# Optimization experiments

Measured on AMD Instinct MI355X. Metric: run time of the kernel, lower is better.

The kernel has to match this reference:

```python
import jax, jax.numpy as jnp
import numpy as np

R, K = 16, 64  # rel_size (heads), key_size (head dim)
LN_EPS = 1e-5


def apply_rope(x, pos):
    # pos: [B,S,1,K], halves are sin/cos; x: [B,S,R,K]
    sin, cos = jnp.split(pos, 2, axis=-1)
    x0, x1 = jnp.split(x, 2, axis=-1)
    return jnp.concatenate([x0 * cos - x1 * sin, x0 * sin + x1 * cos], axis=-1)


def setup_inputs() -> dict:
    key = jax.random.key(0)
    ks = jax.random.split(key, 6)
    B, S, H = 2, 2048, 1024
    x = jax.random.normal(ks[0], (B, S, H), dtype=jnp.float32)
    pos = jax.random.uniform(ks[1], (B, S, 1, K), dtype=jnp.float32)
    W_qkv = jax.random.normal(ks[2], (H, R * K * 3), dtype=jnp.float32) * (H ** -0.5)
    b_qkv = jax.random.normal(ks[3], (R * K * 3,), dtype=jnp.float32) * 0.02
    W_out = jax.random.normal(ks[4], (R * K, H), dtype=jnp.float32) * ((R * K) ** -0.5)
    b_out = jax.random.normal(ks[5], (H,), dtype=jnp.float32) * 0.02
    ln_g = jnp.ones((H,), dtype=jnp.float32)
    ln_b = jnp.zeros((H,), dtype=jnp.float32)
    return {"x": x, "pos": pos, "W_qkv": W_qkv, "b_qkv": b_qkv,
            "W_out": W_out, "b_out": b_out, "ln_g": ln_g, "ln_b": ln_b}


def reference(x, pos, W_qkv, b_qkv, W_out, b_out, ln_g, ln_b):
    B, S, H = x.shape
    qkv = (x @ W_qkv + b_qkv).reshape(B, S, R, 3 * K)
    q, k, v = jnp.split(qkv, 3, axis=-1)  # each [B,S,R,K]
    k = k / jnp.linalg.norm(k, axis=-1, keepdims=True)
    q = apply_rope(q, pos)
    k = apply_rope(k, pos)
    # SDPA with scale=1 (as in the original call)
    scores = jnp.einsum('bqhd,bkhd->bhqk', q, k)
    attn = jax.nn.softmax(scores, axis=-1)
    ctx = jnp.einsum('bhqk,bkhd->bqhd', attn, v).reshape(B, S, R * K)
    postx = ctx @ W_out + b_out
    y = x + postx
    mu = jnp.mean(y, axis=-1, keepdims=True)
    var = jnp.mean(jnp.square(y - mu), axis=-1, keepdims=True)
    return (y - mu) * jax.lax.rsqrt(var + LN_EPS) * ln_g + ln_b
```

## Files before the change

kernel.cpp:

```cpp
#include <hip/hip_runtime.h>


#define B_   2
#define S_   2048
#define H_   1024
#define R_   16
#define BS_  (B_*S_)
#define NQKV 3072
#define LOG2E 1.44269504088896f

typedef float    floatx4 __attribute__((ext_vector_type(4)));
typedef _Float16 half8   __attribute__((ext_vector_type(8)));
typedef _Float16 half4   __attribute__((ext_vector_type(4)));
typedef __fp16   fp16x2  __attribute__((ext_vector_type(2)));

__device__ __forceinline__ float exp2_raw(float x) {
#if __has_builtin(__builtin_amdgcn_exp2f)
    return __builtin_amdgcn_exp2f(x);
#else
    float r;
    asm("v_exp_f32 %0, %1\n\ts_nop 0" : "=v"(r) : "v"(x));
    return r;
#endif
}

__device__ __forceinline__ void gl_lds16(const _Float16* g, _Float16* l) {
    __builtin_amdgcn_global_load_lds(
        (const __attribute__((address_space(1))) unsigned int*)g,
        (__attribute__((address_space(3))) unsigned int*)l, 16, 0, 0);
}

__global__ __launch_bounds__(256) void prep0_kernel(
    const float* __restrict__ x, _Float16* __restrict__ x_h,
    const float* __restrict__ W_qkv, _Float16* __restrict__ wqkv_t,
    const float* __restrict__ W_out, _Float16* __restrict__ wout_t)
{
    __shared__ float tile[32][33];
    int bid = blockIdx.x, tid = threadIdx.x;
    if (bid < 4096) {
        int i = bid * 1024 + tid * 4;
        float4 v = *(const float4*)(x + i);
        half4 h;
        h.x = (_Float16)v.x; h.y = (_Float16)v.y;
        h.z = (_Float16)v.z; h.w = (_Float16)v.w;
        *(half4*)(x_h + i) = h;
        return;
    }
    const float* in; _Float16* out; int rows, cols, bx, by;
    if (bid < 7168) {
        int t = bid - 4096;
        in = W_qkv; out = wqkv_t; rows = H_; cols = NQKV;
        bx = t % 96; by = t / 96;
    } else {
        int t = bid - 7168;
        in = W_out; out = wout_t; rows = H_; cols = H_;
        bx = t & 31; by = t >> 5;
    }
    int cx = bx * 32, ry = by * 32;
    int tx = tid & 31, ty = tid >> 5;
#pragma unroll
    for (int i = 0; i < 32; i += 8)
        tile[ty + i][tx] = in[(size_t)(ry + ty + i) * cols + cx + tx];
    __syncthreads();
#pragma unroll
    for (int i = 0; i < 32; i += 8)
        out[(size_t)(cx + ty + i) * rows + ry + tx] = (_Float16)tile[tx][ty + i];
}

template <bool F16OUT>
__global__ __launch_bounds__(256) void gemm_f16_mfma(
    const _Float16* __restrict__ A, const _Float16* __restrict__ Bt,
    const float* __restrict__ bias, const float* __restrict__ resid,
    float* __restrict__ Cf, _Float16* __restrict__ Ch, int M, int N, int Kd)
{
    __shared__ _Float16 Als[2][4096];
    __shared__ _Float16 Bls[2][4096];
    int tid  = threadIdx.x;
    int lane = tid & 63, w = tid >> 6;
    int wr = w >> 1, wc = w & 1;
    int fr = lane & 15, fq = lane >> 4;
    int m0 = blockIdx.y * 128, n0 = blockIdx.x * 128;

    floatx4 acc[4][4] = {};

    const _Float16* ga[2]; const _Float16* gb[2];
    int loff[2];
#pragma unroll
    for (int i2 = 0; i2 < 2; ++i2) {
        int ch = 2 * w + i2;
        int row = ch * 16 + (lane >> 2), col = (lane & 3) * 8;
        ga[i2] = A  + (size_t)(m0 + row) * Kd + col;
        gb[i2] = Bt + (size_t)(n0 + row) * Kd + col;
        loff[i2] = ch * 512;
    }

    int nIter = Kd >> 5;
#pragma unroll
    for (int i2 = 0; i2 < 2; ++i2) {
        gl_lds16(ga[i2], &Als[0][loff[i2]]);
        gl_lds16(gb[i2], &Bls[0][loff[i2]]);
    }

    for (int it = 0; it < nIter; ++it) {
        int cur = it & 1;
        __syncthreads();
        if (it + 1 < nIter) {
            int k1 = (it + 1) << 5;
#pragma unroll
            for (int i2 = 0; i2 < 2; ++i2) {
                gl_lds16(ga[i2] + k1, &Als[cur ^ 1][loff[i2]]);
                gl_lds16(gb[i2] + k1, &Bls[cur ^ 1][loff[i2]]);
            }
        }
        const _Float16* Ab = Als[cur];
        const _Float16* Bb = Bls[cur];
        half8 af[4], bf[4];
#pragma unroll
        for (int i = 0; i < 4; ++i)
            af[i] = *(const half8*)(Ab + (wr * 64 + i * 16 + fr) * 32 + fq * 8);
#pragma unroll
        for (int j = 0; j < 4; ++j)
            bf[j] = *(const half8*)(Bb + (wc * 64 + j * 16 + fr) * 32 + fq * 8);
#pragma unroll
        for (int i = 0; i < 4; ++i)
#pragma unroll
            for (int j = 0; j < 4; ++j)
                acc[i][j] = __builtin_amdgcn_mfma_f32_16x16x32_f16(
                    af[i], bf[j], acc[i][j], 0, 0, 0);
    }

#pragma unroll
    for (int i = 0; i < 4; ++i)
#pragma unroll
        for (int j = 0; j < 4; ++j)
#pragma unroll
            for (int r2 = 0; r2 < 4; ++r2) {
                int row = m0 + wr * 64 + i * 16 + fq * 4 + r2;
                int col = n0 + wc * 64 + j * 16 + fr;
                float v = acc[i][j][r2] + bias[col];
                if constexpr (F16OUT) {
                    Ch[(size_t)row * N + col] = (_Float16)v;
                } else {
                    if (resid) v += resid[(size_t)row * N + col];
                    Cf[(size_t)row * N + col] = v;
                }
            }
}

__global__ __launch_bounds__(256) void prep1_kernel(
    const _Float16* __restrict__ qkvh, const float* __restrict__ pos,
    _Float16* __restrict__ qt, _Float16* __restrict__ kt,
    _Float16* __restrict__ vt2)
{
    __shared__ float tile[64][65];
    int head = blockIdx.x, tau = blockIdx.y;
    int s0 = tau * 64;
    int b = head >> 4, rh = head & 15;
    int lane = threadIdx.x & 63, w = threadIdx.x >> 6;

#pragma unroll
    for (int si = w; si < 64; si += 4)
        tile[si][lane] =
            (float)qkvh[(size_t)(b * S_ + s0 + si) * NQKV + rh * 192 + 128 + lane];
    __syncthreads();
    {
        int P = lane;
        int op = P >> 3;
        int hi = (P >> 2) & 1, lo = P & 3;
#pragma unroll
        for (int d = w; d < 64; d += 4) {
            int ol = op ^ (d & 7);
            int key = 32 * (ol >> 2) + 16 * hi + 4 * (ol & 3) + lo;
            vt2[(((size_t)head * 32 + tau) * 64 + d) * 64 + P] = (_Float16)tile[key][d];
        }
    }

    for (int i = 0; i < 16; ++i) {
        int s = s0 + w * 16 + i;
        int bs = b * S_ + s;
        const _Float16* base = qkvh + (size_t)bs * NQKV + rh * 192;
        float qv = (float)base[lane];
        float kv = (float)base[64 + lane];

        float ss = kv * kv;
#pragma unroll
        for (int off = 32; off > 0; off >>= 1) ss += __shfl_xor(ss, off);
        kv *= rsqrtf(ss);

        int j = lane & 31;
        float sn = pos[(size_t)bs * 64 + j];
        float cs = pos[(size_t)bs * 64 + 32 + j];
        float qp = __shfl_xor(qv, 32);
        float kp = __shfl_xor(kv, 32);
        float qo, ko;
        if (lane < 32) { qo = qv * cs - qp * sn; ko = kv * cs - kp * sn; }
        else           { qo = qp * sn + qv * cs; ko = kp * sn + kv * cs; }

        size_t oidx = ((size_t)head * S_ + s) * 64 + lane;
        qt[oidx] = (_Float16)(qo * LOG2E);
        kt[oidx] = (_Float16)ko;
    }
}

__global__ __launch_bounds__(256) void attn_mfma_kernel(
    const _Float16* __restrict__ qt, const _Float16* __restrict__ kt,
    const _Float16* __restrict__ vt2, _Float16* __restrict__ ctx)
{
    __shared__ _Float16 Kls[64 * 64];
    __shared__ _Float16 Vls[64 * 64];

    int head = blockIdx.x, q0 = blockIdx.y * 128;
    int b = head >> 4, rh = head & 15;
    int tid = threadIdx.x, lane = tid & 63, w = tid >> 6;
    int g = lane >> 4, c = lane & 15;

    half8 qf[2][2];
    float mL[2], l_s[2] = {0.f, 0.f};
#pragma unroll
    for (int qg = 0; qg < 2; ++qg) {
        const _Float16* qp =
            qt + ((size_t)head * S_ + q0 + w * 32 + qg * 16 + c) * 64 + 8 * g;
        qf[qg][0] = *(const half8*)qp;
        qf[qg][1] = *(const half8*)(qp + 32);
        float qq = 0.f;
#pragma unroll
        for (int i = 0; i < 8; ++i) {
            float a = (float)qf[qg][0][i], b2 = (float)qf[qg][1][i];
            qq += a * a + b2 * b2;
        }
        qq += __shfl_xor(qq, 16);
        qq += __shfl_xor(qq, 32);
        mL[qg] = sqrtf(qq);
    }

    floatx4 o_acc[2][4] = {};

    const _Float16* kg[2]; const _Float16* vg[2];
    _Float16 *kl_[2], *vl_[2];
#pragma unroll
    for (int i2 = 0; i2 < 2; ++i2) {
        int ch = 2 * w + i2;
        int krow = ch * 8 + (lane >> 3);
        int koct = (lane & 7) ^ (lane >> 3);
        kg[i2] = kt + ((size_t)head * S_ + krow) * 64 + koct * 8;
        kl_[i2] = Kls + ch * 512;
        vg[i2] = vt2 + ((size_t)head * 32) * 4096 + ch * 512 + lane * 8;
        vl_[i2] = Vls + ch * 512;
    }

    int co = c & 7;

    for (int j0 = 0; j0 < S_; j0 += 64) {
        __syncthreads();
#pragma unroll
        for (int i2 = 0; i2 < 2; ++i2) {
            gl_lds16(kg[i2] + (size_t)j0 * 64, kl_[i2]);
            gl_lds16(vg[i2] + (size_t)(j0 >> 6) * 4096, vl_[i2]);
        }
        __syncthreads();

        half8 kfr[8];
#pragma unroll
        for (int t = 0; t < 4; ++t) {
            const _Float16* krow = Kls + (16 * t + c) * 64;
            kfr[2 * t]     = *(const half8*)(krow + ((g) ^ co) * 8);
            kfr[2 * t + 1] = *(const half8*)(krow + ((4 + g) ^ co) * 8);
        }

        union { half8 v; fp16x2 h2[4]; } pf[2][2];
#pragma unroll
        for (int qg = 0; qg < 2; ++qg) {
            float negm = -mL[qg];
            floatx4 zinit = {negm, negm, negm, negm};
            floatx4 sacc[4];
#pragma unroll
            for (int t = 0; t < 4; ++t) {
                floatx4 z = zinit;
                z = __builtin_amdgcn_mfma_f32_16x16x32_f16(
                    kfr[2 * t], qf[qg][0], z, 0, 0, 0);
                z = __builtin_amdgcn_mfma_f32_16x16x32_f16(
                    kfr[2 * t + 1], qf[qg][1], z, 0, 0, 0);
                sacc[t] = z;
            }
            float ps = 0.f;
#pragma unroll
            for (int t = 0; t < 4; ++t)
#pragma unroll
                for (int r = 0; r < 4; ++r) {
                    float p = exp2_raw(sacc[t][r]);
                    sacc[t][r] = p;
                    ps += p;
                }
            l_s[qg] += ps;
            pf[qg][0].h2[0] = __builtin_amdgcn_cvt_pkrtz(sacc[0][0], sacc[0][1]);
            pf[qg][0].h2[1] = __builtin_amdgcn_cvt_pkrtz(sacc[0][2], sacc[0][3]);
            pf[qg][0].h2[2] = __builtin_amdgcn_cvt_pkrtz(sacc[1][0], sacc[1][1]);
            pf[qg][0].h2[3] = __builtin_amdgcn_cvt_pkrtz(sacc[1][2], sacc[1][3]);
            pf[qg][1].h2[0] = __builtin_amdgcn_cvt_pkrtz(sacc[2][0], sacc[2][1]);
            pf[qg][1].h2[1] = __builtin_amdgcn_cvt_pkrtz(sacc[2][2], sacc[2][3]);
            pf[qg][1].h2[2] = __builtin_amdgcn_cvt_pkrtz(sacc[3][0], sacc[3][1]);
            pf[qg][1].h2[3] = __builtin_amdgcn_cvt_pkrtz(sacc[3][2], sacc[3][3]);
        }

#pragma unroll
        for (int t = 0; t < 4; ++t) {
            const _Float16* vrow = Vls + (16 * t + c) * 64;
            half8 v0 = *(const half8*)(vrow + ((g) ^ co) * 8);
            half8 v1 = *(const half8*)(vrow + ((4 + g) ^ co) * 8);
#pragma unroll
            for (int qg = 0; qg < 2; ++qg) {
                o_acc[qg][t] = __builtin_amdgcn_mfma_f32_16x16x32_f16(
                    v0, pf[qg][0].v, o_acc[qg][t], 0, 0, 0);
                o_acc[qg][t] = __builtin_amdgcn_mfma_f32_16x16x32_f16(
                    v1, pf[qg][1].v, o_acc[qg][t], 0, 0, 0);
            }
        }
    }

#pragma unroll
    for (int qg = 0; qg < 2; ++qg) {
        float lt = l_s[qg];
        lt += __shfl_xor(lt, 16);
        lt += __shfl_xor(lt, 32);
        float inv = 1.f / lt;
        size_t rowbase =
            ((size_t)(b * S_ + q0 + w * 32 + qg * 16 + c)) * 1024 + rh * 64;
#pragma unroll
        for (int t = 0; t < 4; ++t) {
            union { half4 v; fp16x2 h2[2]; } e;
            e.h2[0] = __builtin_amdgcn_cvt_pkrtz(o_acc[qg][t][0] * inv,
                                                 o_acc[qg][t][1] * inv);
            e.h2[1] = __builtin_amdgcn_cvt_pkrtz(o_acc[qg][t][2] * inv,
                                                 o_acc[qg][t][3] * inv);
            *(half4*)(ctx + rowbase + 16 * t + 4 * g) = e.v;
        }
    }
}

__global__ __launch_bounds__(256) void ln_kernel(
    float* __restrict__ y, const float* __restrict__ g, const float* __restrict__ bb)
{
    int row = blockIdx.x, tid = threadIdx.x;
    float* p = y + (size_t)row * 1024;
    float4 v = ((const float4*)p)[tid];
    float sum = v.x + v.y + v.z + v.w;
    float sq  = v.x*v.x + v.y*v.y + v.z*v.z + v.w*v.w;
#pragma unroll
    for (int off = 32; off > 0; off >>= 1) {
        sum += __shfl_xor(sum, off);
        sq  += __shfl_xor(sq,  off);
    }
    __shared__ float rs[4], rq[4];
    int w = tid >> 6;
    if ((tid & 63) == 0) { rs[w] = sum; rq[w] = sq; }
    __syncthreads();
    sum = rs[0] + rs[1] + rs[2] + rs[3];
    sq  = rq[0] + rq[1] + rq[2] + rq[3];
    float mean = sum * (1.f / 1024.f);
    float var  = sq * (1.f / 1024.f) - mean * mean;
    float inv  = rsqrtf(var + 1e-5f);
    float4 gv = ((const float4*)g)[tid];
    float4 bv = ((const float4*)bb)[tid];
    v.x = (v.x - mean) * inv * gv.x + bv.x;
    v.y = (v.y - mean) * inv * gv.y + bv.y;
    v.z = (v.z - mean) * inv * gv.z + bv.z;
    v.w = (v.w - mean) * inv * gv.w + bv.w;
    ((float4*)p)[tid] = v;
}

extern "C" void kernel_launch(void* const* d_in, const int* in_sizes, int n_in,
                              void* d_out, int out_size, void* d_ws, size_t ws_size,
                              hipStream_t stream)
{
    const float* x     = (const float*)d_in[0];
    const float* pos   = (const float*)d_in[1];
    const float* W_qkv = (const float*)d_in[2];
    const float* b_qkv = (const float*)d_in[3];
    const float* W_out = (const float*)d_in[4];
    const float* b_out = (const float*)d_in[5];
    const float* ln_g  = (const float*)d_in[6];
    const float* ln_b  = (const float*)d_in[7];
    float* out = (float*)d_out;

    char* ws = (char*)d_ws;
    _Float16* x_h    = (_Float16*)(ws);
    _Float16* wqkv_t = (_Float16*)(ws + ((size_t)8  << 20));
    _Float16* wout_t = (_Float16*)(ws + ((size_t)14 << 20));
    _Float16* qkvh   = (_Float16*)(ws + ((size_t)16 << 20));
    _Float16* qt_h   = (_Float16*)(ws + ((size_t)40 << 20));
    _Float16* kt_h   = (_Float16*)(ws + ((size_t)48 << 20));
    _Float16* vt2_h  = (_Float16*)(ws + ((size_t)56 << 20));
    _Float16* ctx_h  = (_Float16*)(ws + ((size_t)64 << 20));

    prep0_kernel<<<8192, 256, 0, stream>>>(x, x_h, W_qkv, wqkv_t, W_out, wout_t);

    gemm_f16_mfma<true><<<dim3(NQKV / 128, BS_ / 128), 256, 0, stream>>>(
        x_h, wqkv_t, b_qkv, nullptr, nullptr, qkvh, BS_, NQKV, H_);

    prep1_kernel<<<dim3(32, 32), 256, 0, stream>>>(qkvh, pos, qt_h, kt_h, vt2_h);

    attn_mfma_kernel<<<dim3(32, 16), 256, 0, stream>>>(qt_h, kt_h, vt2_h, ctx_h);

    gemm_f16_mfma<false><<<dim3(H_ / 128, BS_ / 128), 256, 0, stream>>>(
        ctx_h, wout_t, b_out, x, out, nullptr, BS_, H_, H_);

    ln_kernel<<<BS_, 256, 0, stream>>>(out, ln_g, ln_b);
}
```

Measured before the change: 229.4 us.

## Double-buffer K/V tiles in LDS to overlap loads with attention compute

```diff
diff --git a/kernel.cpp b/kernel.cpp
--- a/kernel.cpp
+++ b/kernel.cpp
@@ -14,15 +14,11 @@
 typedef _Float16 half4   __attribute__((ext_vector_type(4)));
 typedef __fp16   fp16x2  __attribute__((ext_vector_type(2)));
 
-__device__ __forceinline__ float exp2_raw(float x) {
 #if __has_builtin(__builtin_amdgcn_exp2f)
-    return __builtin_amdgcn_exp2f(x);
+#define EXP2(x) __builtin_amdgcn_exp2f(x)
 #else
-    float r;
-    asm("v_exp_f32 %0, %1\n\ts_nop 0" : "=v"(r) : "v"(x));
-    return r;
+#define EXP2(x) exp2f(x)
 #endif
-}
 
 __device__ __forceinline__ void gl_lds16(const _Float16* g, _Float16* l) {
     __builtin_amdgcn_global_load_lds(
@@ -206,8 +202,8 @@
     const _Float16* __restrict__ qt, const _Float16* __restrict__ kt,
     const _Float16* __restrict__ vt2, _Float16* __restrict__ ctx)
 {
-    __shared__ _Float16 Kls[64 * 64];
-    __shared__ _Float16 Vls[64 * 64];
+    __shared__ _Float16 Kls[2][4096];
+    __shared__ _Float16 Vls[2][4096];
 
     int head = blockIdx.x, q0 = blockIdx.y * 128;
     int b = head >> 4, rh = head & 15;
@@ -236,33 +232,42 @@
     floatx4 o_acc[2][4] = {};
 
     const _Float16* kg[2]; const _Float16* vg[2];
-    _Float16 *kl_[2], *vl_[2];
+    int loff[2];
 #pragma unroll
     for (int i2 = 0; i2 < 2; ++i2) {
         int ch = 2 * w + i2;
         int krow = ch * 8 + (lane >> 3);
         int koct = (lane & 7) ^ (lane >> 3);
         kg[i2] = kt + ((size_t)head * S_ + krow) * 64 + koct * 8;
-        kl_[i2] = Kls + ch * 512;
         vg[i2] = vt2 + ((size_t)head * 32) * 4096 + ch * 512 + lane * 8;
-        vl_[i2] = Vls + ch * 512;
+        loff[i2] = ch * 512;
     }
 
     int co = c & 7;
 
-    for (int j0 = 0; j0 < S_; j0 += 64) {
+#pragma unroll
+    for (int i2 = 0; i2 < 2; ++i2) {
+        gl_lds16(kg[i2], &Kls[0][loff[i2]]);
+        gl_lds16(vg[i2], &Vls[0][loff[i2]]);
+    }
+
+    for (int jt = 0; jt < 32; ++jt) {
+        int cur = jt & 1;
         __syncthreads();
-#pragma unroll
-        for (int i2 = 0; i2 < 2; ++i2) {
-            gl_lds16(kg[i2] + (size_t)j0 * 64, kl_[i2]);
-            gl_lds16(vg[i2] + (size_t)(j0 >> 6) * 4096, vl_[i2]);
-        }
-        __syncthreads();
+        if (jt + 1 < 32) {
+#pragma unroll
+            for (int i2 = 0; i2 < 2; ++i2) {
+                gl_lds16(kg[i2] + (size_t)(jt + 1) * 4096, &Kls[cur ^ 1][loff[i2]]);
+                gl_lds16(vg[i2] + (size_t)(jt + 1) * 4096, &Vls[cur ^ 1][loff[i2]]);
+            }
+        }
+        const _Float16* Kbuf = Kls[cur];
+        const _Float16* Vbuf = Vls[cur];
 
         half8 kfr[8];
 #pragma unroll
         for (int t = 0; t < 4; ++t) {
-            const _Float16* krow = Kls + (16 * t + c) * 64;
+            const _Float16* krow = Kbuf + (16 * t + c) * 64;
             kfr[2 * t]     = *(const half8*)(krow + ((g) ^ co) * 8);
             kfr[2 * t + 1] = *(const half8*)(krow + ((4 + g) ^ co) * 8);
         }
@@ -270,24 +275,22 @@
         union { half8 v; fp16x2 h2[4]; } pf[2][2];
 #pragma unroll
         for (int qg = 0; qg < 2; ++qg) {
-            float negm = -mL[qg];
-            floatx4 zinit = {negm, negm, negm, negm};
             floatx4 sacc[4];
 #pragma unroll
             for (int t = 0; t < 4; ++t) {
-                floatx4 z = zinit;
+                floatx4 z = {};
                 z = __builtin_amdgcn_mfma_f32_16x16x32_f16(
                     kfr[2 * t], qf[qg][0], z, 0, 0, 0);
                 z = __builtin_amdgcn_mfma_f32_16x16x32_f16(
                     kfr[2 * t + 1], qf[qg][1], z, 0, 0, 0);
                 sacc[t] = z;
             }
-            float ps = 0.f;
+            float mLq = mL[qg], ps = 0.f;
 #pragma unroll
             for (int t = 0; t < 4; ++t)
 #pragma unroll
                 for (int r = 0; r < 4; ++r) {
-                    float p = exp2_raw(sacc[t][r]);
+                    float p = EXP2(sacc[t][r] - mLq);
                     sacc[t][r] = p;
                     ps += p;
                 }
@@ -304,7 +307,7 @@
 
 #pragma unroll
         for (int t = 0; t < 4; ++t) {
-            const _Float16* vrow = Vls + (16 * t + c) * 64;
+            const _Float16* vrow = Vbuf + (16 * t + c) * 64;
             half8 v0 = *(const half8*)(vrow + ((g) ^ co) * 8);
             half8 v1 = *(const half8*)(vrow + ((4 + g) ^ co) * 8);
 #pragma unroll
```

New measurement: 228.7 us. Within noise of the previous version (-0.3%).
